# Kernel tuning notes

Hardware: AMD Instinct MI355X
Metric: run time of the kernel (lower is better)

The kernel has to match this reference:

```python
import jax, jax.numpy as jnp
import numpy as np

B, N, D, L, T = 64, 64, 128, 4, 10  # batch, atoms, hidden_dim, n_layers, n_atom_types
EPS = 1e-5


def setup_inputs() -> dict:
    key = jax.random.key(0)
    ks = jax.random.split(key, 10)
    def rn(k, shape, s=0.05):
        return jax.random.normal(k, shape, jnp.float32) * s
    return dict(
        positions=jax.random.normal(ks[0], (B, N, 3), jnp.float32),
        atomic_numbers=jax.random.randint(ks[1], (B, N), 0, T),
        embed=rn(ks[2], (T, D)),
        edge_w1=rn(ks[3], (L, 2 * D + 1, D)), edge_b1=jnp.zeros((L, D), jnp.float32),
        edge_w2=rn(ks[4], (L, D, D)), edge_b2=jnp.zeros((L, D), jnp.float32),
        node_w1=rn(ks[5], (L, 2 * D, D)), node_b1=jnp.zeros((L, D), jnp.float32),
        node_w2=rn(ks[6], (L, D, D)), node_b2=jnp.zeros((L, D), jnp.float32),
        ln_g=jnp.ones((L, D), jnp.float32), ln_b=jnp.zeros((L, D), jnp.float32),
        out_w=rn(ks[7], (D, 3)), out_b=jnp.zeros((3,), jnp.float32),
    )


def _layer(h, dist_sq, ew1, eb1, ew2, eb2, nw1, nb1, nw2, nb2, g, b):
    # edge_mlp first linear on cat([h_i, h_j, dist_sq]) == h@Wa (bcast over j)
    # + h@Wb (bcast over i) + dist_sq * w_d, avoiding materializing the concat.
    wa, wb, wd = ew1[:D], ew1[D:2 * D], ew1[2 * D]
    pre = (h @ wa)[:, :, None, :] + (h @ wb)[:, None, :, :] + dist_sq * wd + eb1  # [B,N,N,D]
    m_ij = jax.nn.silu(jax.nn.silu(pre) @ ew2 + eb2)
    m_i = m_ij.mean(axis=2)  # mean over j -> [B,N,D]
    # node_mlp on cat([h, m_i]) split the same way; dropout is eval-mode identity.
    h_out = jax.nn.silu(h @ nw1[:D] + m_i @ nw1[D:] + nb1) @ nw2 + nb2
    x = h + h_out
    mu = x.mean(-1, keepdims=True)
    var = ((x - mu) ** 2).mean(-1, keepdims=True)
    return (x - mu) / jnp.sqrt(var + EPS) * g + b


def reference(positions, atomic_numbers, embed, edge_w1, edge_b1, edge_w2, edge_b2,
              node_w1, node_b1, node_w2, node_b2, ln_g, ln_b, out_w, out_b):
    h = embed[atomic_numbers]  # [B,N,D]
    diff = positions[:, :, None, :] - positions[:, None, :, :]
    dist_sq = (diff ** 2).sum(-1, keepdims=True)  # [B,N,N,1]
    for i in range(L):
        h = _layer(h, dist_sq, edge_w1[i], edge_b1[i], edge_w2[i], edge_b2[i],
                   node_w1[i], node_b1[i], node_w2[i], node_b2[i], ln_g[i], ln_b[i])
    return h @ out_w + out_b  # [B,N,3]
```

## Files before the change

### kernel.cpp

```cpp
#include <hip/hip_runtime.h>
#include <hip/hip_fp16.h>


typedef _Float16 f16;
typedef _Float16 f16x4 __attribute__((ext_vector_type(4)));
typedef _Float16 f16x8 __attribute__((ext_vector_type(8)));
typedef float f32x4 __attribute__((ext_vector_type(4)));

union H2x4 { f16x8 v; __half2 h[4]; };

__device__ __forceinline__ float bf2f(unsigned short u) {
    union { unsigned int i; float f; } v; v.i = ((unsigned int)u) << 16; return v.f;
}
__device__ __forceinline__ unsigned short f2bf(float f) {
    union { float f; unsigned int i; } v; v.f = f;
    unsigned int x = v.i;
    return (unsigned short)((x + 0x7fffu + ((x >> 16) & 1u)) >> 16);
}
__device__ __forceinline__ float silu_f(float x) {
    float e = __builtin_amdgcn_exp2f(-1.44269504088896f * x);
    return x * __builtin_amdgcn_rcpf(1.0f + e);
}
__device__ __forceinline__ __half2 silu_h2(__half2 x, __half2 kf, __half2 one2) {
    __half2 e = h2exp2(__hmul2(x, kf));
    return __hmul2(x, h2rcp(__hadd2(one2, e)));
}

struct Ptrs { const void* p[14]; };

__device__ __forceinline__ float ldf(const void* p, int i, int bf) {
    return bf ? bf2f(((const unsigned short*)p)[i]) : ((const float*)p)[i];
}

#define FRAG_TOTAL 49152
#define ELEM_TOTAL 393216
#define SMALL_TOTAL 17539

__global__ __launch_bounds__(256) void prep_kernel(
    Ptrs ptrs, f16* dst, float* sc)
{
    __shared__ int flgsh;
    int t = threadIdx.x;
    if (t < 64) {
        int ex = (((const unsigned short*)ptrs.p[0])[t * 2] >> 7) & 0xFF;
        unsigned long long m = __ballot(ex >= 110 && ex <= 135);
        if (t == 0) flgsh = (__popcll(m) >= 40) ? 1 : 0;
    }
    __syncthreads();
    int bf = flgsh;

    int gid = blockIdx.x * 256 + t;
    if (gid < ELEM_TOTAL) {
        int f = gid >> 3, j = gid & 7;
        int lay = f / 12288;
        int r   = f % 12288;
        const void* src; int base, rowoff = 0, r2;
        if (r < 6144) {
            int mat = r >> 11; r2 = r & 2047;
            if (mat == 0)      { src = ptrs.p[2]; base = lay * 32896; }
            else if (mat == 1) { src = ptrs.p[2]; base = lay * 32896; rowoff = 128; }
            else               { src = ptrs.p[4]; base = lay * 16384; }
        } else if (r < 10240) {
            r2 = r - 6144; src = ptrs.p[6]; base = lay * 32768;
        } else {
            r2 = r - 10240; src = ptrs.p[8]; base = lay * 16384;
        }
        int s = r2 >> 9, c = (r2 >> 6) & 7, l = r2 & 63;
        int row = rowoff + s * 32 + ((l >> 4) << 3) + j;
        int col = (c << 4) + (l & 15);
        dst[gid] = (f16)ldf(src, base + row * 128 + col, bf);
    } else {
        int sid = gid - ELEM_TOTAL;
        if (sid >= SMALL_TOTAL) return;
        const void* src; int i;
        if      (sid < 12288) { src = ptrs.p[0]; i = sid; }
        else if (sid < 13568) { src = ptrs.p[1]; i = sid - 12288; }
        else if (sid < 14080) { int k = sid - 13568;
                                src = ptrs.p[2]; i = (k >> 7) * 32896 + 32768 + (k & 127); }
        else if (sid < 14592) { src = ptrs.p[3];  i = sid - 14080; }
        else if (sid < 15104) { src = ptrs.p[5];  i = sid - 14592; }
        else if (sid < 15616) { src = ptrs.p[7];  i = sid - 15104; }
        else if (sid < 16128) { src = ptrs.p[9];  i = sid - 15616; }
        else if (sid < 16640) { src = ptrs.p[10]; i = sid - 16128; }
        else if (sid < 17152) { src = ptrs.p[11]; i = sid - 16640; }
        else if (sid < 17536) { src = ptrs.p[12]; i = sid - 17152; }
        else                  { src = ptrs.p[13]; i = sid - 17536; }
        sc[sid] = ldf(src, i, bf);
    }
}

__global__ __launch_bounds__(512) void embed_ab_kernel(
    const int* an, const float* sc, const f16* wa, const f16* wb,
    const float* eb1C, f16* h16, f16* a16, f16* b16)
{
    int t = threadIdx.x;
    int w = t >> 6, lane = t & 63;
    int row0 = blockIdx.x << 4;
    int m_ = lane & 15, q_ = lane >> 4;
    const float* emb = sc + 12288;
    int a = an[row0 + m_];
    a = a < 0 ? 0 : (a > 9 ? 9 : a);
    f16x8 afrag[4];
#pragma unroll
    for (int s = 0; s < 4; s++) {
        f32x4 u0 = *(const f32x4*)(emb + a * 128 + s * 32 + q_ * 8);
        f32x4 u1 = *(const f32x4*)(emb + a * 128 + s * 32 + q_ * 8 + 4);
        f16x8 hv;
#pragma unroll
        for (int e = 0; e < 4; e++) { hv[e] = (f16)u0[e]; hv[e + 4] = (f16)u1[e]; }
        afrag[s] = hv;
        if (w == 0)
            *(f16x8*)(h16 + (row0 + m_) * 128 + s * 32 + q_ * 8) = hv;
    }
    int c = w;
#pragma unroll
    for (int mat = 0; mat < 2; mat++) {
        const f16* W = mat ? wb : wa;
        f16* out     = mat ? b16 : a16;
        float init = mat ? 0.0f : eb1C[c * 16 + m_];
        f32x4 acc = { init, init, init, init };
#pragma unroll
        for (int s = 0; s < 4; s++) {
            f16x8 bfr = *(const f16x8*)(W + ((s * 8 + c) * 64 + lane) * 8);
            acc = __builtin_amdgcn_mfma_f32_16x16x32_f16(afrag[s], bfr, acc, 0, 0, 0);
        }
#pragma unroll
        for (int r = 0; r < 4; r++)
            out[(row0 + q_ * 4 + r) * 128 + c * 16 + m_] = (f16)acc[r];
    }
}

__global__ __launch_bounds__(256) void edge_kernel(
    const float* sc, const f16* a16, const f16* b16,
    const f16* ew2_swz, const float* eb2C, const float* wdC, f16* m_out)
{
    __shared__ f16 Wlds[8192];
    __shared__ f16 S[64 * 136];
    __shared__ __half2 wd2_sh[64];
    __shared__ float dsq_sh[64];
    __shared__ float msum[256];

    int t  = threadIdx.x;
    int ig = blockIdx.x;
    int b  = ig >> 6;
    const float* posC = sc;
    int lane = t & 63, w = t >> 6;
    int wr = w & 1, wc = w >> 1;

#pragma unroll
    for (int k = 0; k < 4; k++) {
        int idx = (k * 256 + t) * 8;
        *(f16x8*)(Wlds + idx) = *(const f16x8*)(ew2_swz + idx);
    }
    f16x8 bfB[2][4];
#pragma unroll
    for (int s2 = 0; s2 < 2; s2++)
#pragma unroll
        for (int c = 0; c < 4; c++)
            bfB[s2][c] = *(const f16x8*)(ew2_swz +
                (((s2 + 2) * 8 + wc * 4 + c) * 64 + lane) * 8);

    if (t >= 64 && t < 128) {
        int u = t - 64;
        wd2_sh[u] = __floats2half2_rn(wdC[2 * u], wdC[2 * u + 1]);
    }
    if (t < 64) {
        float xi = posC[ig * 3 + 0], yi = posC[ig * 3 + 1], zi = posC[ig * 3 + 2];
        int jg = b * 64 + t;
        float dx = xi - posC[jg * 3 + 0];
        float dy = yi - posC[jg * 3 + 1];
        float dz = zi - posC[jg * 3 + 2];
        dsq_sh[t] = dx * dx + dy * dy + dz * dz;
    }
    __syncthreads();

    {
        int j  = t >> 2;
        int cb = (t & 3) * 32;
        float dsf = dsq_sh[j];
        __half dh = __float2half_rn(dsf);
        __half2 ds2 = __halves2half2(dh, dh);
        __half2 kf   = __floats2half2_rn(-1.44269504f, -1.44269504f);
        __half2 one2 = __floats2half2_rn(1.0f, 1.0f);
        H2x4 a_r[4], wd_r[4];
#pragma unroll
        for (int k = 0; k < 4; k++) {
            a_r[k].v  = *(const f16x8*)(a16 + ig * 128 + cb + k * 8);
            wd_r[k].v = *(const f16x8*)((const f16*)wd2_sh + cb + k * 8);
        }
#pragma unroll
        for (int k = 0; k < 4; k++) {
            H2x4 bv, sv;
            bv.v = *(const f16x8*)(b16 + (b * 64 + j) * 128 + cb + k * 8);
#pragma unroll
            for (int e = 0; e < 4; e++) {
                __half2 pre = __hfma2(ds2, wd_r[k].h[e],
                                      __hadd2(a_r[k].h[e], bv.h[e]));
                sv.h[e] = silu_h2(pre, kf, one2);
            }
            *(f16x8*)(S + j * 136 + cb + k * 8) = sv.v;
        }
    }
    __syncthreads();

    int m_ = lane & 15, q_ = lane >> 4;
    f32x4 acc[4][2];
#pragma unroll
    for (int c = 0; c < 4; c++) {
        float e = eb2C[(wc * 4 + c) * 16 + m_];
        acc[c][0] = (f32x4){ e, e, e, e };
        acc[c][1] = acc[c][0];
    }
#pragma unroll
    for (int s = 0; s < 2; s++) {
        f16x8 bfr[4];
#pragma unroll
        for (int c = 0; c < 4; c++)
            bfr[c] = *(const f16x8*)(Wlds + ((s * 8 + wc * 4 + c) * 64 + lane) * 8);
#pragma unroll
        for (int mb = 0; mb < 2; mb++) {
            f16x8 af = *(const f16x8*)(S + ((wr * 2 + mb) * 16 + m_) * 136 + s * 32 + q_ * 8);
#pragma unroll
            for (int c = 0; c < 4; c++)
                acc[c][mb] = __builtin_amdgcn_mfma_f32_16x16x32_f16(af, bfr[c], acc[c][mb], 0, 0, 0);
        }
    }
#pragma unroll
    for (int s2 = 0; s2 < 2; s2++) {
#pragma unroll
        for (int mb = 0; mb < 2; mb++) {
            f16x8 af = *(const f16x8*)(S + ((wr * 2 + mb) * 16 + m_) * 136 + (s2 + 2) * 32 + q_ * 8);
#pragma unroll
            for (int c = 0; c < 4; c++)
                acc[c][mb] = __builtin_amdgcn_mfma_f32_16x16x32_f16(af, bfB[s2][c], acc[c][mb], 0, 0, 0);
        }
    }
    float scv4[4];
#pragma unroll
    for (int c = 0; c < 4; c++) {
        float scv = 0.0f;
#pragma unroll
        for (int mb = 0; mb < 2; mb++)
#pragma unroll
            for (int r = 0; r < 4; r++)
                scv += silu_f(acc[c][mb][r]);
        scv += __shfl_xor(scv, 16);
        scv += __shfl_xor(scv, 32);
        scv4[c] = scv;
    }
    if (lane < 16) {
#pragma unroll
        for (int c = 0; c < 4; c++)
            msum[wr * 128 + (wc * 4 + c) * 16 + lane] = scv4[c];
    }
    __syncthreads();
    if (t < 128) {
        float mv = (msum[t] + msum[128 + t]) * (1.0f / 64.0f);
        m_out[ig * 128 + t] = (f16)mv;
    }
}

__global__ __launch_bounds__(512) void node_mid_kernel(
    const f16* h16, const f16* m16, const f16* nw1s, const f16* nw2s,
    const float* nb1C, const float* nb2C, const float* lngC, const float* lnbC,
    const f16* waN, const f16* wbN, const float* eb1N,
    f16* a16, f16* b16)
{
    __shared__ f16 relay[16 * 136];
    __shared__ float s1sh[8][16], s2sh[8][16];
    int t = threadIdx.x;
    int w = t >> 6, lane = t & 63;
    int row0 = blockIdx.x << 4;
    int m_ = lane & 15, q_ = lane >> 4;
    int c = w;

    f16x8 af[8];
#pragma unroll
    for (int s = 0; s < 4; s++) {
        af[s]     = *(const f16x8*)(h16 + (row0 + m_) * 128 + s * 32 + q_ * 8);
        af[s + 4] = *(const f16x8*)(m16 + (row0 + m_) * 128 + s * 32 + q_ * 8);
    }
    {
        float e = nb1C[c * 16 + m_];
        f32x4 acc = { e, e, e, e };
#pragma unroll
        for (int s = 0; s < 8; s++) {
            f16x8 bfr = *(const f16x8*)(nw1s + ((s * 8 + c) * 64 + lane) * 8);
            acc = __builtin_amdgcn_mfma_f32_16x16x32_f16(af[s], bfr, acc, 0, 0, 0);
        }
#pragma unroll
        for (int r = 0; r < 4; r++)
            relay[(q_ * 4 + r) * 136 + c * 16 + m_] = (f16)silu_f(acc[r]);
    }
    __syncthreads();
    f16x8 uf[4];
#pragma unroll
    for (int s = 0; s < 4; s++)
        uf[s] = *(const f16x8*)(relay + m_ * 136 + s * 32 + q_ * 8);
    float x[4];
    {
        float e = nb2C[c * 16 + m_];
        f32x4 acc = { e, e, e, e };
#pragma unroll
        for (int s = 0; s < 4; s++) {
            f16x8 bfr = *(const f16x8*)(nw2s + ((s * 8 + c) * 64 + lane) * 8);
            acc = __builtin_amdgcn_mfma_f32_16x16x32_f16(uf[s], bfr, acc, 0, 0, 0);
        }
#pragma unroll
        for (int r = 0; r < 4; r++)
            x[r] = acc[r] + (float)h16[(row0 + q_ * 4 + r) * 128 + c * 16 + m_];
    }
    float s1p[4], s2p[4];
#pragma unroll
    for (int r = 0; r < 4; r++) {
        s1p[r] = x[r];
        s2p[r] = x[r] * x[r];
    }
#pragma unroll
    for (int msk = 1; msk < 16; msk <<= 1)
#pragma unroll
        for (int r = 0; r < 4; r++) {
            s1p[r] += __shfl_xor(s1p[r], msk);
            s2p[r] += __shfl_xor(s2p[r], msk);
        }
    if (m_ == 0)
#pragma unroll
        for (int r = 0; r < 4; r++) {
            s1sh[w][q_ * 4 + r] = s1p[r];
            s2sh[w][q_ * 4 + r] = s2p[r];
        }
    __syncthreads();
    float mu[4], rs[4];
#pragma unroll
    for (int r = 0; r < 4; r++) {
        int row = q_ * 4 + r;
        float S1 = 0.0f, S2 = 0.0f;
#pragma unroll
        for (int w2 = 0; w2 < 8; w2++) { S1 += s1sh[w2][row]; S2 += s2sh[w2][row]; }
        mu[r] = S1 * (1.0f / 128.0f);
        float var = S2 * (1.0f / 128.0f) - mu[r] * mu[r];
        rs[r] = rsqrtf(var + 1e-5f);
    }
#pragma unroll
    for (int r = 0; r < 4; r++) {
        int col = c * 16 + m_;
        int row = row0 + q_ * 4 + r;
        float y = (x[r] - mu[r]) * rs[r] * lngC[col] + lnbC[col];
        ((f16*)h16)[row * 128 + col] = (f16)y;
        relay[(q_ * 4 + r) * 136 + col] = (f16)y;
    }
    __syncthreads();
    f16x8 hf[4];
#pragma unroll
    for (int s = 0; s < 4; s++)
        hf[s] = *(const f16x8*)(relay + m_ * 136 + s * 32 + q_ * 8);
#pragma unroll
    for (int mat = 0; mat < 2; mat++) {
        const f16* W = mat ? wbN : waN;
        f16* out     = mat ? b16 : a16;
        float init = mat ? 0.0f : eb1N[c * 16 + m_];
        f32x4 acc = { init, init, init, init };
#pragma unroll
        for (int s = 0; s < 4; s++) {
            f16x8 bfr = *(const f16x8*)(W + ((s * 8 + c) * 64 + lane) * 8);
            acc = __builtin_amdgcn_mfma_f32_16x16x32_f16(hf[s], bfr, acc, 0, 0, 0);
        }
#pragma unroll
        for (int r = 0; r < 4; r++)
            out[(row0 + q_ * 4 + r) * 128 + c * 16 + m_] = (f16)acc[r];
    }
}

__global__ __launch_bounds__(512) void node_final_kernel(
    const void* pos_raw, const f16* h16, const f16* m16,
    const f16* nw1s, const f16* nw2s,
    const float* nb1C, const float* nb2C, const float* lngC, const float* lnbC,
    const float* owC, const float* obC, void* out)
{
    __shared__ f16 relay[16 * 136];
    __shared__ float s1sh[8][16], s2sh[8][16];
    __shared__ float psh[8][16][3];
    __shared__ int flgsh;
    int t = threadIdx.x;
    int w = t >> 6, lane = t & 63;
    int row0 = blockIdx.x << 4;
    int m_ = lane & 15, q_ = lane >> 4;
    int c = w;

    if (t < 64) {
        int ex = (((const unsigned short*)pos_raw)[t * 2] >> 7) & 0xFF;
        unsigned long long mk = __ballot(ex >= 110 && ex <= 135);
        if (t == 0) flgsh = (__popcll(mk) >= 40) ? 1 : 0;
    }

    f16x8 af[8];
#pragma unroll
    for (int s = 0; s < 4; s++) {
        af[s]     = *(const f16x8*)(h16 + (row0 + m_) * 128 + s * 32 + q_ * 8);
        af[s + 4] = *(const f16x8*)(m16 + (row0 + m_) * 128 + s * 32 + q_ * 8);
    }
    {
        float e = nb1C[c * 16 + m_];
        f32x4 acc = { e, e, e, e };
#pragma unroll
        for (int s = 0; s < 8; s++) {
            f16x8 bfr = *(const f16x8*)(nw1s + ((s * 8 + c) * 64 + lane) * 8);
            acc = __builtin_amdgcn_mfma_f32_16x16x32_f16(af[s], bfr, acc, 0, 0, 0);
        }
#pragma unroll
        for (int r = 0; r < 4; r++)
            relay[(q_ * 4 + r) * 136 + c * 16 + m_] = (f16)silu_f(acc[r]);
    }
    __syncthreads();
    f16x8 uf[4];
#pragma unroll
    for (int s = 0; s < 4; s++)
        uf[s] = *(const f16x8*)(relay + m_ * 136 + s * 32 + q_ * 8);
    float x[4];
    {
        float e = nb2C[c * 16 + m_];
        f32x4 acc = { e, e, e, e };
#pragma unroll
        for (int s = 0; s < 4; s++) {
            f16x8 bfr = *(const f16x8*)(nw2s + ((s * 8 + c) * 64 + lane) * 8);
            acc = __builtin_amdgcn_mfma_f32_16x16x32_f16(uf[s], bfr, acc, 0, 0, 0);
        }
#pragma unroll
        for (int r = 0; r < 4; r++)
            x[r] = acc[r] + (float)h16[(row0 + q_ * 4 + r) * 128 + c * 16 + m_];
    }
    float s1p[4], s2p[4];
#pragma unroll
    for (int r = 0; r < 4; r++) {
        s1p[r] = x[r];
        s2p[r] = x[r] * x[r];
    }
#pragma unroll
    for (int msk = 1; msk < 16; msk <<= 1)
#pragma unroll
        for (int r = 0; r < 4; r++) {
            s1p[r] += __shfl_xor(s1p[r], msk);
            s2p[r] += __shfl_xor(s2p[r], msk);
        }
    if (m_ == 0)
#pragma unroll
        for (int r = 0; r < 4; r++) {
            s1sh[w][q_ * 4 + r] = s1p[r];
            s2sh[w][q_ * 4 + r] = s2p[r];
        }
    __syncthreads();
    float p[3][4];
#pragma unroll
    for (int r = 0; r < 4; r++) {
        int row = q_ * 4 + r;
        float S1 = 0.0f, S2 = 0.0f;
#pragma unroll
        for (int w2 = 0; w2 < 8; w2++) { S1 += s1sh[w2][row]; S2 += s2sh[w2][row]; }
        float mu = S1 * (1.0f / 128.0f);
        float var = S2 * (1.0f / 128.0f) - mu * mu;
        float rs = rsqrtf(var + 1e-5f);
        int col = c * 16 + m_;
        float y = (x[r] - mu) * rs * lngC[col] + lnbC[col];
        p[0][r] = y * owC[col * 3 + 0];
        p[1][r] = y * owC[col * 3 + 1];
        p[2][r] = y * owC[col * 3 + 2];
    }
#pragma unroll
    for (int msk = 1; msk < 16; msk <<= 1)
#pragma unroll
        for (int k = 0; k < 3; k++)
#pragma unroll
            for (int r = 0; r < 4; r++)
                p[k][r] += __shfl_xor(p[k][r], msk);
    if (m_ == 0)
#pragma unroll
        for (int r = 0; r < 4; r++)
#pragma unroll
            for (int k = 0; k < 3; k++)
                psh[w][q_ * 4 + r][k] = p[k][r];
    __syncthreads();
    if (t < 16) {
        int row = row0 + t;
        int bf = flgsh;
#pragma unroll
        for (int k = 0; k < 3; k++) {
            float v = obC[k];
#pragma unroll
            for (int w2 = 0; w2 < 8; w2++) v += psh[w2][t][k];
            if (bf) ((unsigned short*)out)[row * 3 + k] = f2bf(v);
            else    ((float*)out)[row * 3 + k] = v;
        }
    }
}

extern "C" void kernel_launch(void* const* d_in, const int* in_sizes, int n_in,
                              void* d_out, int out_size, void* d_ws, size_t ws_size,
                              hipStream_t stream)
{
    const int* an = (const int*)d_in[1];

    char* ws = (char*)d_ws;
    float* sc   = (float*)(ws + 1024);
    f16*   Wswz = (f16*)(ws + (128u << 10));
    f16*   h16  = (f16*)(ws + (1u << 20));
    f16*   a16  = (f16*)(ws + (2u << 20));
    f16*   b16  = (f16*)(ws + (3u << 20));
    f16*   m16  = (f16*)(ws + (4u << 20));

    Ptrs ptrs;
    const int src_idx[14] = {0, 2, 3, 4, 5, 6, 7, 8, 9, 10, 11, 12, 13, 14};
    for (int k = 0; k < 14; k++) ptrs.p[k] = d_in[src_idx[k]];

    prep_kernel<<<1605, 256, 0, stream>>>(ptrs, Wswz, sc);
    embed_ab_kernel<<<256, 512, 0, stream>>>(an, sc, Wswz, Wswz + 16384,
                                             sc + 14080, h16, a16, b16);
    for (int lay = 0; lay < 4; lay++) {
        const f16* wl = Wswz + lay * 98304;
        const float* wdC  = sc + 13568 + lay * 128;
        const float* eb2C = sc + 14592 + lay * 128;
        const float* nb1C = sc + 15104 + lay * 128;
        const float* nb2C = sc + 15616 + lay * 128;
        const float* lngC = sc + 16128 + lay * 128;
        const float* lnbC = sc + 16640 + lay * 128;

        edge_kernel<<<4096, 256, 0, stream>>>(sc, a16, b16, wl + 32768,
                                              eb2C, wdC, m16);
        if (lay < 3) {
            const f16* wlN = Wswz + (lay + 1) * 98304;
            node_mid_kernel<<<256, 512, 0, stream>>>(
                h16, m16, wl + 49152, wl + 81920, nb1C, nb2C, lngC, lnbC,
                wlN, wlN + 16384, sc + 14080 + (lay + 1) * 128, a16, b16);
        } else {
            node_final_kernel<<<256, 512, 0, stream>>>(
                d_in[0], h16, m16, wl + 49152, wl + 81920,
                nb1C, nb2C, lngC, lnbC,
                sc + 17152, sc + 17536, d_out);
        }
    }
}
```

Baseline: 216.0 us.

## Fuse embed, edge, and node layers into one persistent kernel with per-batch flags

Replaces the embed, per-layer edge, and node kernels with a single 256-block persistent kernel. Each block owns 16 rows of one molecule and runs all four layers, keeping h, a, and m in LDS. Blocks of the same batch exchange the b projection through double-buffered global memory and synchronise with atomic per-batch flags. This removes eight kernel launches and the global round trips for m/h/a, but edge work drops from 4096 blocks to 256 blocks, which lowers parallelism and adds spin-wait synchronisation between co-resident blocks.

```diff
diff --git a/kernel.cpp b/kernel.cpp
--- a/kernel.cpp
+++ b/kernel.cpp
@@ -3,7 +3,6 @@
 
 
 typedef _Float16 f16;
-typedef _Float16 f16x4 __attribute__((ext_vector_type(4)));
 typedef _Float16 f16x8 __attribute__((ext_vector_type(8)));
 typedef float f32x4 __attribute__((ext_vector_type(4)));
 
@@ -32,15 +31,15 @@
     return bf ? bf2f(((const unsigned short*)p)[i]) : ((const float*)p)[i];
 }
 
-#define FRAG_TOTAL 49152
 #define ELEM_TOTAL 393216
 #define SMALL_TOTAL 17539
 
 __global__ __launch_bounds__(256) void prep_kernel(
-    Ptrs ptrs, f16* dst, float* sc)
+    Ptrs ptrs, f16* dst, float* sc, int* flags)
 {
     __shared__ int flgsh;
     int t = threadIdx.x;
+    if (blockIdx.x == 0 && t < 64) flags[t] = 0;
     if (t < 64) {
         int ex = (((const unsigned short*)ptrs.p[0])[t * 2] >> 7) & 0xFF;
         unsigned long long m = __ballot(ex >= 110 && ex <= 135);
@@ -89,452 +88,325 @@
     }
 }
 
-__global__ __launch_bounds__(512) void embed_ab_kernel(
-    const int* an, const float* sc, const f16* wa, const f16* wb,
-    const float* eb1C, f16* h16, f16* a16, f16* b16)
+__global__ __launch_bounds__(512) void net_kernel(
+    const void* pos_raw, const int* an, const float* sc, const f16* Wswz,
+    f16* b0, f16* b1, int* flags, void* out)
 {
+    __shared__ f16 S[2][64 * 136];
+    __shared__ f16 a_lds[16 * 136];
+    __shared__ f16 h_lds[16 * 136];
+    __shared__ f16 m_lds[16 * 136];
+    __shared__ __half dsq2[16][64];
+    __shared__ __half2 wd2_sh[64];
+    __shared__ float s1sh[8][16], s2sh[8][16];
+    __shared__ int flgsh;
+
     int t = threadIdx.x;
     int w = t >> 6, lane = t & 63;
-    int row0 = blockIdx.x << 4;
-    int m_ = lane & 15, q_ = lane >> 4;
-    const float* emb = sc + 12288;
-    int a = an[row0 + m_];
-    a = a < 0 ? 0 : (a > 9 ? 9 : a);
-    f16x8 afrag[4];
-#pragma unroll
-    for (int s = 0; s < 4; s++) {
-        f32x4 u0 = *(const f32x4*)(emb + a * 128 + s * 32 + q_ * 8);
-        f32x4 u1 = *(const f32x4*)(emb + a * 128 + s * 32 + q_ * 8 + 4);
-        f16x8 hv;
-#pragma unroll
-        for (int e = 0; e < 4; e++) { hv[e] = (f16)u0[e]; hv[e + 4] = (f16)u1[e]; }
-        afrag[s] = hv;
-        if (w == 0)
-            *(f16x8*)(h16 + (row0 + m_) * 128 + s * 32 + q_ * 8) = hv;
-    }
-    int c = w;
-#pragma unroll
-    for (int mat = 0; mat < 2; mat++) {
-        const f16* W = mat ? wb : wa;
-        f16* out     = mat ? b16 : a16;
-        float init = mat ? 0.0f : eb1C[c * 16 + m_];
-        f32x4 acc = { init, init, init, init };
-#pragma unroll
-        for (int s = 0; s < 4; s++) {
-            f16x8 bfr = *(const f16x8*)(W + ((s * 8 + c) * 64 + lane) * 8);
-            acc = __builtin_amdgcn_mfma_f32_16x16x32_f16(afrag[s], bfr, acc, 0, 0, 0);
-        }
-#pragma unroll
-        for (int r = 0; r < 4; r++)
-            out[(row0 + q_ * 4 + r) * 128 + c * 16 + m_] = (f16)acc[r];
-    }
-}
-
-__global__ __launch_bounds__(256) void edge_kernel(
-    const float* sc, const f16* a16, const f16* b16,
-    const f16* ew2_swz, const float* eb2C, const float* wdC, f16* m_out)
-{
-    __shared__ f16 Wlds[8192];
-    __shared__ f16 S[64 * 136];
-    __shared__ __half2 wd2_sh[64];
-    __shared__ float dsq_sh[64];
-    __shared__ float msum[256];
-
-    int t  = threadIdx.x;
-    int ig = blockIdx.x;
-    int b  = ig >> 6;
-    const float* posC = sc;
-    int lane = t & 63, w = t >> 6;
-    int wr = w & 1, wc = w >> 1;
-
-#pragma unroll
-    for (int k = 0; k < 4; k++) {
-        int idx = (k * 256 + t) * 8;
-        *(f16x8*)(Wlds + idx) = *(const f16x8*)(ew2_swz + idx);
-    }
-    f16x8 bfB[2][4];
-#pragma unroll
-    for (int s2 = 0; s2 < 2; s2++)
-#pragma unroll
-        for (int c = 0; c < 4; c++)
-            bfB[s2][c] = *(const f16x8*)(ew2_swz +
-                (((s2 + 2) * 8 + wc * 4 + c) * 64 + lane) * 8);
-
-    if (t >= 64 && t < 128) {
-        int u = t - 64;
-        wd2_sh[u] = __floats2half2_rn(wdC[2 * u], wdC[2 * u + 1]);
-    }
-    if (t < 64) {
-        float xi = posC[ig * 3 + 0], yi = posC[ig * 3 + 1], zi = posC[ig * 3 + 2];
-        int jg = b * 64 + t;
-        float dx = xi - posC[jg * 3 + 0];
-        float dy = yi - posC[jg * 3 + 1];
-        float dz = zi - posC[jg * 3 + 2];
-        dsq_sh[t] = dx * dx + dy * dy + dz * dz;
-    }
-    __syncthreads();
-
-    {
-        int j  = t >> 2;
-        int cb = (t & 3) * 32;
-        float dsf = dsq_sh[j];
-        __half dh = __float2half_rn(dsf);
-        __half2 ds2 = __halves2half2(dh, dh);
-        __half2 kf   = __floats2half2_rn(-1.44269504f, -1.44269504f);
-        __half2 one2 = __floats2half2_rn(1.0f, 1.0f);
-        H2x4 a_r[4], wd_r[4];
-#pragma unroll
-        for (int k = 0; k < 4; k++) {
-            a_r[k].v  = *(const f16x8*)(a16 + ig * 128 + cb + k * 8);
-            wd_r[k].v = *(const f16x8*)((const f16*)wd2_sh + cb + k * 8);
-        }
-#pragma unroll
-        for (int k = 0; k < 4; k++) {
-            H2x4 bv, sv;
-            bv.v = *(const f16x8*)(b16 + (b * 64 + j) * 128 + cb + k * 8);
-#pragma unroll
-            for (int e = 0; e < 4; e++) {
-                __half2 pre = __hfma2(ds2, wd_r[k].h[e],
-                                      __hadd2(a_r[k].h[e], bv.h[e]));
-                sv.h[e] = silu_h2(pre, kf, one2);
-            }
-            *(f16x8*)(S + j * 136 + cb + k * 8) = sv.v;
-        }
-    }
-    __syncthreads();
-
-    int m_ = lane & 15, q_ = lane >> 4;
-    f32x4 acc[4][2];
-#pragma unroll
-    for (int c = 0; c < 4; c++) {
-        float e = eb2C[(wc * 4 + c) * 16 + m_];
-        acc[c][0] = (f32x4){ e, e, e, e };
-        acc[c][1] = acc[c][0];
-    }
-#pragma unroll
-    for (int s = 0; s < 2; s++) {
-        f16x8 bfr[4];
-#pragma unroll
-        for (int c = 0; c < 4; c++)
-            bfr[c] = *(const f16x8*)(Wlds + ((s * 8 + wc * 4 + c) * 64 + lane) * 8);
-#pragma unroll
-        for (int mb = 0; mb < 2; mb++) {
-            f16x8 af = *(const f16x8*)(S + ((wr * 2 + mb) * 16 + m_) * 136 + s * 32 + q_ * 8);
-#pragma unroll
-            for (int c = 0; c < 4; c++)
-                acc[c][mb] = __builtin_amdgcn_mfma_f32_16x16x32_f16(af, bfr[c], acc[c][mb], 0, 0, 0);
-        }
-    }
-#pragma unroll
-    for (int s2 = 0; s2 < 2; s2++) {
-#pragma unroll
-        for (int mb = 0; mb < 2; mb++) {
-            f16x8 af = *(const f16x8*)(S + ((wr * 2 + mb) * 16 + m_) * 136 + (s2 + 2) * 32 + q_ * 8);
-#pragma unroll
-            for (int c = 0; c < 4; c++)
-                acc[c][mb] = __builtin_amdgcn_mfma_f32_16x16x32_f16(af, bfB[s2][c], acc[c][mb], 0, 0, 0);
-        }
-    }
-    float scv4[4];
-#pragma unroll
-    for (int c = 0; c < 4; c++) {
-        float scv = 0.0f;
-#pragma unroll
-        for (int mb = 0; mb < 2; mb++)
-#pragma unroll
-            for (int r = 0; r < 4; r++)
-                scv += silu_f(acc[c][mb][r]);
-        scv += __shfl_xor(scv, 16);
-        scv += __shfl_xor(scv, 32);
-        scv4[c] = scv;
-    }
-    if (lane < 16) {
-#pragma unroll
-        for (int c = 0; c < 4; c++)
-            msum[wr * 128 + (wc * 4 + c) * 16 + lane] = scv4[c];
-    }
-    __syncthreads();
-    if (t < 128) {
-        float mv = (msum[t] + msum[128 + t]) * (1.0f / 64.0f);
-        m_out[ig * 128 + t] = (f16)mv;
-    }
-}
-
-__global__ __launch_bounds__(512) void node_mid_kernel(
-    const f16* h16, const f16* m16, const f16* nw1s, const f16* nw2s,
-    const float* nb1C, const float* nb2C, const float* lngC, const float* lnbC,
-    const f16* waN, const f16* wbN, const float* eb1N,
-    f16* a16, f16* b16)
-{
-    __shared__ f16 relay[16 * 136];
-    __shared__ float s1sh[8][16], s2sh[8][16];
-    int t = threadIdx.x;
-    int w = t >> 6, lane = t & 63;
-    int row0 = blockIdx.x << 4;
     int m_ = lane & 15, q_ = lane >> 4;
     int c = w;
-
-    f16x8 af[8];
-#pragma unroll
-    for (int s = 0; s < 4; s++) {
-        af[s]     = *(const f16x8*)(h16 + (row0 + m_) * 128 + s * 32 + q_ * 8);
-        af[s + 4] = *(const f16x8*)(m16 + (row0 + m_) * 128 + s * 32 + q_ * 8);
-    }
-    {
-        float e = nb1C[c * 16 + m_];
-        f32x4 acc = { e, e, e, e };
-#pragma unroll
-        for (int s = 0; s < 8; s++) {
-            f16x8 bfr = *(const f16x8*)(nw1s + ((s * 8 + c) * 64 + lane) * 8);
-            acc = __builtin_amdgcn_mfma_f32_16x16x32_f16(af[s], bfr, acc, 0, 0, 0);
-        }
-#pragma unroll
-        for (int r = 0; r < 4; r++)
-            relay[(q_ * 4 + r) * 136 + c * 16 + m_] = (f16)silu_f(acc[r]);
-    }
-    __syncthreads();
-    f16x8 uf[4];
-#pragma unroll
-    for (int s = 0; s < 4; s++)
-        uf[s] = *(const f16x8*)(relay + m_ * 136 + s * 32 + q_ * 8);
-    float x[4];
-    {
-        float e = nb2C[c * 16 + m_];
-        f32x4 acc = { e, e, e, e };
-#pragma unroll
-        for (int s = 0; s < 4; s++) {
-            f16x8 bfr = *(const f16x8*)(nw2s + ((s * 8 + c) * 64 + lane) * 8);
-            acc = __builtin_amdgcn_mfma_f32_16x16x32_f16(uf[s], bfr, acc, 0, 0, 0);
-        }
-#pragma unroll
-        for (int r = 0; r < 4; r++)
-            x[r] = acc[r] + (float)h16[(row0 + q_ * 4 + r) * 128 + c * 16 + m_];
-    }
-    float s1p[4], s2p[4];
-#pragma unroll
-    for (int r = 0; r < 4; r++) {
-        s1p[r] = x[r];
-        s2p[r] = x[r] * x[r];
-    }
-#pragma unroll
-    for (int msk = 1; msk < 16; msk <<= 1)
-#pragma unroll
-        for (int r = 0; r < 4; r++) {
-            s1p[r] += __shfl_xor(s1p[r], msk);
-            s2p[r] += __shfl_xor(s2p[r], msk);
-        }
-    if (m_ == 0)
-#pragma unroll
-        for (int r = 0; r < 4; r++) {
-            s1sh[w][q_ * 4 + r] = s1p[r];
-            s2sh[w][q_ * 4 + r] = s2p[r];
-        }
-    __syncthreads();
-    float mu[4], rs[4];
-#pragma unroll
-    for (int r = 0; r < 4; r++) {
-        int row = q_ * 4 + r;
-        float S1 = 0.0f, S2 = 0.0f;
-#pragma unroll
-        for (int w2 = 0; w2 < 8; w2++) { S1 += s1sh[w2][row]; S2 += s2sh[w2][row]; }
-        mu[r] = S1 * (1.0f / 128.0f);
-        float var = S2 * (1.0f / 128.0f) - mu[r] * mu[r];
-        rs[r] = rsqrtf(var + 1e-5f);
-    }
-#pragma unroll
-    for (int r = 0; r < 4; r++) {
-        int col = c * 16 + m_;
-        int row = row0 + q_ * 4 + r;
-        float y = (x[r] - mu[r]) * rs[r] * lngC[col] + lnbC[col];
-        ((f16*)h16)[row * 128 + col] = (f16)y;
-        relay[(q_ * 4 + r) * 136 + col] = (f16)y;
-    }
-    __syncthreads();
-    f16x8 hf[4];
-#pragma unroll
-    for (int s = 0; s < 4; s++)
-        hf[s] = *(const f16x8*)(relay + m_ * 136 + s * 32 + q_ * 8);
-#pragma unroll
-    for (int mat = 0; mat < 2; mat++) {
-        const f16* W = mat ? wbN : waN;
-        f16* out     = mat ? b16 : a16;
-        float init = mat ? 0.0f : eb1N[c * 16 + m_];
-        f32x4 acc = { init, init, init, init };
-#pragma unroll
-        for (int s = 0; s < 4; s++) {
-            f16x8 bfr = *(const f16x8*)(W + ((s * 8 + c) * 64 + lane) * 8);
-            acc = __builtin_amdgcn_mfma_f32_16x16x32_f16(hf[s], bfr, acc, 0, 0, 0);
-        }
-#pragma unroll
-        for (int r = 0; r < 4; r++)
-            out[(row0 + q_ * 4 + r) * 128 + c * 16 + m_] = (f16)acc[r];
-    }
-}
-
-__global__ __launch_bounds__(512) void node_final_kernel(
-    const void* pos_raw, const f16* h16, const f16* m16,
-    const f16* nw1s, const f16* nw2s,
-    const float* nb1C, const float* nb2C, const float* lngC, const float* lnbC,
-    const float* owC, const float* obC, void* out)
-{
-    __shared__ f16 relay[16 * 136];
-    __shared__ float s1sh[8][16], s2sh[8][16];
-    __shared__ float psh[8][16][3];
-    __shared__ int flgsh;
-    int t = threadIdx.x;
-    int w = t >> 6, lane = t & 63;
-    int row0 = blockIdx.x << 4;
-    int m_ = lane & 15, q_ = lane >> 4;
-    int c = w;
+    int b  = blockIdx.x >> 2;
+    int r0 = b * 64 + (blockIdx.x & 3) * 16;
+    const float* posC = sc;
 
     if (t < 64) {
         int ex = (((const unsigned short*)pos_raw)[t * 2] >> 7) & 0xFF;
         unsigned long long mk = __ballot(ex >= 110 && ex <= 135);
         if (t == 0) flgsh = (__popcll(mk) >= 40) ? 1 : 0;
     }
-
-    f16x8 af[8];
-#pragma unroll
-    for (int s = 0; s < 4; s++) {
-        af[s]     = *(const f16x8*)(h16 + (row0 + m_) * 128 + s * 32 + q_ * 8);
-        af[s + 4] = *(const f16x8*)(m16 + (row0 + m_) * 128 + s * 32 + q_ * 8);
-    }
+    for (int k = t; k < 1024; k += 512) {
+        int ii = k >> 6, j = k & 63;
+        int gi = r0 + ii, gj = b * 64 + j;
+        float dx = posC[gi * 3 + 0] - posC[gj * 3 + 0];
+        float dy = posC[gi * 3 + 1] - posC[gj * 3 + 1];
+        float dz = posC[gi * 3 + 2] - posC[gj * 3 + 2];
+        dsq2[ii][j] = __float2half_rn(dx * dx + dy * dy + dz * dz);
+    }
+
     {
-        float e = nb1C[c * 16 + m_];
-        f32x4 acc = { e, e, e, e };
-#pragma unroll
-        for (int s = 0; s < 8; s++) {
-            f16x8 bfr = *(const f16x8*)(nw1s + ((s * 8 + c) * 64 + lane) * 8);
-            acc = __builtin_amdgcn_mfma_f32_16x16x32_f16(af[s], bfr, acc, 0, 0, 0);
-        }
-#pragma unroll
-        for (int r = 0; r < 4; r++)
-            relay[(q_ * 4 + r) * 136 + c * 16 + m_] = (f16)silu_f(acc[r]);
+        const float* emb  = sc + 12288;
+        const float* eb1C = sc + 14080;
+        int a = an[r0 + m_];
+        a = a < 0 ? 0 : (a > 9 ? 9 : a);
+        f16x8 afrag[4];
+#pragma unroll
+        for (int s = 0; s < 4; s++) {
+            f32x4 u0 = *(const f32x4*)(emb + a * 128 + s * 32 + q_ * 8);
+            f32x4 u1 = *(const f32x4*)(emb + a * 128 + s * 32 + q_ * 8 + 4);
+            f16x8 hv;
+#pragma unroll
+            for (int e = 0; e < 4; e++) { hv[e] = (f16)u0[e]; hv[e + 4] = (f16)u1[e]; }
+            afrag[s] = hv;
+            if (w == 0)
+                *(f16x8*)(h_lds + m_ * 136 + s * 32 + q_ * 8) = hv;
+        }
+#pragma unroll
+        for (int mat = 0; mat < 2; mat++) {
+            const f16* W = mat ? (Wswz + 16384) : Wswz;
+            float init = mat ? 0.0f : eb1C[c * 16 + m_];
+            f32x4 acc = { init, init, init, init };
+#pragma unroll
+            for (int s = 0; s < 4; s++) {
+                f16x8 bfv = *(const f16x8*)(W + ((s * 8 + c) * 64 + lane) * 8);
+                acc = __builtin_amdgcn_mfma_f32_16x16x32_f16(afrag[s], bfv, acc, 0, 0, 0);
+            }
+#pragma unroll
+            for (int r = 0; r < 4; r++) {
+                if (mat == 0)
+                    a_lds[(q_ * 4 + r) * 136 + c * 16 + m_] = (f16)acc[r];
+                else
+                    b0[(r0 + q_ * 4 + r) * 128 + c * 16 + m_] = (f16)acc[r];
+            }
+        }
     }
     __syncthreads();
-    f16x8 uf[4];
-#pragma unroll
-    for (int s = 0; s < 4; s++)
-        uf[s] = *(const f16x8*)(relay + m_ * 136 + s * 32 + q_ * 8);
-    float x[4];
-    {
-        float e = nb2C[c * 16 + m_];
-        f32x4 acc = { e, e, e, e };
-#pragma unroll
-        for (int s = 0; s < 4; s++) {
-            f16x8 bfr = *(const f16x8*)(nw2s + ((s * 8 + c) * 64 + lane) * 8);
-            acc = __builtin_amdgcn_mfma_f32_16x16x32_f16(uf[s], bfr, acc, 0, 0, 0);
-        }
-#pragma unroll
-        for (int r = 0; r < 4; r++)
-            x[r] = acc[r] + (float)h16[(row0 + q_ * 4 + r) * 128 + c * 16 + m_];
-    }
-    float s1p[4], s2p[4];
-#pragma unroll
-    for (int r = 0; r < 4; r++) {
-        s1p[r] = x[r];
-        s2p[r] = x[r] * x[r];
-    }
-#pragma unroll
-    for (int msk = 1; msk < 16; msk <<= 1)
-#pragma unroll
-        for (int r = 0; r < 4; r++) {
-            s1p[r] += __shfl_xor(s1p[r], msk);
-            s2p[r] += __shfl_xor(s2p[r], msk);
-        }
-    if (m_ == 0)
-#pragma unroll
-        for (int r = 0; r < 4; r++) {
-            s1sh[w][q_ * 4 + r] = s1p[r];
-            s2sh[w][q_ * 4 + r] = s2p[r];
-        }
-    __syncthreads();
-    float p[3][4];
-#pragma unroll
-    for (int r = 0; r < 4; r++) {
-        int row = q_ * 4 + r;
-        float S1 = 0.0f, S2 = 0.0f;
-#pragma unroll
-        for (int w2 = 0; w2 < 8; w2++) { S1 += s1sh[w2][row]; S2 += s2sh[w2][row]; }
-        float mu = S1 * (1.0f / 128.0f);
-        float var = S2 * (1.0f / 128.0f) - mu * mu;
-        float rs = rsqrtf(var + 1e-5f);
-        int col = c * 16 + m_;
-        float y = (x[r] - mu) * rs * lngC[col] + lnbC[col];
-        p[0][r] = y * owC[col * 3 + 0];
-        p[1][r] = y * owC[col * 3 + 1];
-        p[2][r] = y * owC[col * 3 + 2];
-    }
-#pragma unroll
-    for (int msk = 1; msk < 16; msk <<= 1)
-#pragma unroll
-        for (int k = 0; k < 3; k++)
-#pragma unroll
-            for (int r = 0; r < 4; r++)
-                p[k][r] += __shfl_xor(p[k][r], msk);
-    if (m_ == 0)
-#pragma unroll
-        for (int r = 0; r < 4; r++)
-#pragma unroll
-            for (int k = 0; k < 3; k++)
-                psh[w][q_ * 4 + r][k] = p[k][r];
-    __syncthreads();
-    if (t < 16) {
-        int row = row0 + t;
-        int bf = flgsh;
-#pragma unroll
-        for (int k = 0; k < 3; k++) {
-            float v = obC[k];
-#pragma unroll
-            for (int w2 = 0; w2 < 8; w2++) v += psh[w2][t][k];
-            if (bf) ((unsigned short*)out)[row * 3 + k] = f2bf(v);
-            else    ((float*)out)[row * 3 + k] = v;
-        }
-    }
-}
-
-extern "C" void kernel_launch(void* const* d_in, const int* in_sizes, int n_in,
-                              void* d_out, int out_size, void* d_ws, size_t ws_size,
-                              hipStream_t stream)
-{
-    const int* an = (const int*)d_in[1];
-
-    char* ws = (char*)d_ws;
-    float* sc   = (float*)(ws + 1024);
-    f16*   Wswz = (f16*)(ws + (128u << 10));
-    f16*   h16  = (f16*)(ws + (1u << 20));
-    f16*   a16  = (f16*)(ws + (2u << 20));
-    f16*   b16  = (f16*)(ws + (3u << 20));
-    f16*   m16  = (f16*)(ws + (4u << 20));
-
-    Ptrs ptrs;
-    const int src_idx[14] = {0, 2, 3, 4, 5, 6, 7, 8, 9, 10, 11, 12, 13, 14};
-    for (int k = 0; k < 14; k++) ptrs.p[k] = d_in[src_idx[k]];
-
-    prep_kernel<<<1605, 256, 0, stream>>>(ptrs, Wswz, sc);
-    embed_ab_kernel<<<256, 512, 0, stream>>>(an, sc, Wswz, Wswz + 16384,
-                                             sc + 14080, h16, a16, b16);
+    if (t == 0) {
+        __threadfence();
+        __hip_atomic_fetch_add(&flags[b], 1, __ATOMIC_RELEASE,
+                               __HIP_MEMORY_SCOPE_AGENT);
+    }
+
     for (int lay = 0; lay < 4; lay++) {
-        const f16* wl = Wswz + lay * 98304;
+        const f16* wl   = Wswz + lay * 98304;
+        const f16* ew2s = wl + 32768;
+        const f16* nw1s = wl + 49152;
+        const f16* nw2s = wl + 81920;
         const float* wdC  = sc + 13568 + lay * 128;
         const float* eb2C = sc + 14592 + lay * 128;
         const float* nb1C = sc + 15104 + lay * 128;
         const float* nb2C = sc + 15616 + lay * 128;
         const float* lngC = sc + 16128 + lay * 128;
         const float* lnbC = sc + 16640 + lay * 128;
-
-        edge_kernel<<<4096, 256, 0, stream>>>(sc, a16, b16, wl + 32768,
-                                              eb2C, wdC, m16);
+        const f16* bcur = (lay & 1) ? b1 : b0;
+        f16*       bnxt = (lay & 1) ? b0 : b1;
+
+        if (t == 0) {
+            int target = 4 * (lay + 1);
+            int spins = 0;
+            while (__hip_atomic_load(&flags[b], __ATOMIC_ACQUIRE,
+                                     __HIP_MEMORY_SCOPE_AGENT) < target) {
+                __builtin_amdgcn_s_sleep(8);
+                if (++spins > (1 << 20)) break;
+            }
+        }
+        __syncthreads();
+
+        if (t < 64) wd2_sh[t] = __floats2half2_rn(wdC[2 * t], wdC[2 * t + 1]);
+        f16x8 bfr[4];
+#pragma unroll
+        for (int s = 0; s < 4; s++)
+            bfr[s] = *(const f16x8*)(ew2s + ((s * 8 + c) * 64 + lane) * 8);
+        __syncthreads();
+
+        float eb2v = eb2C[c * 16 + m_];
+        const __half2 kf   = __floats2half2_rn(-1.44269504f, -1.44269504f);
+        const __half2 one2 = __floats2half2_rn(1.0f, 1.0f);
+        for (int i = 0; i < 16; i++) {
+            f16* Sc = S[i & 1];
+#pragma unroll
+            for (int k = 0; k < 2; k++) {
+                int chunk = t + 512 * k;
+                int row = chunk >> 4, col = (chunk & 15) * 8;
+                __half dh = dsq2[i][row];
+                __half2 ds2 = __halves2half2(dh, dh);
+                H2x4 av, bv, wv, sv;
+                av.v = *(const f16x8*)(a_lds + i * 136 + col);
+                bv.v = *(const f16x8*)(bcur + (b * 64 + row) * 128 + col);
+                wv.v = *(const f16x8*)((const f16*)wd2_sh + col);
+#pragma unroll
+                for (int e = 0; e < 4; e++) {
+                    __half2 pre = __hfma2(ds2, wv.h[e], __hadd2(av.h[e], bv.h[e]));
+                    sv.h[e] = silu_h2(pre, kf, one2);
+                }
+                *(f16x8*)(Sc + row * 136 + col) = sv.v;
+            }
+            __syncthreads();
+            f32x4 acc[4];
+#pragma unroll
+            for (int mb = 0; mb < 4; mb++) acc[mb] = (f32x4){ eb2v, eb2v, eb2v, eb2v };
+#pragma unroll
+            for (int s = 0; s < 4; s++)
+#pragma unroll
+                for (int mb = 0; mb < 4; mb++) {
+                    f16x8 af = *(const f16x8*)(Sc + (mb * 16 + m_) * 136 + s * 32 + q_ * 8);
+                    acc[mb] = __builtin_amdgcn_mfma_f32_16x16x32_f16(af, bfr[s], acc[mb], 0, 0, 0);
+                }
+            float scv = 0.0f;
+#pragma unroll
+            for (int mb = 0; mb < 4; mb++)
+#pragma unroll
+                for (int r = 0; r < 4; r++)
+                    scv += silu_f(acc[mb][r]);
+            scv += __shfl_xor(scv, 16);
+            scv += __shfl_xor(scv, 32);
+            if (lane < 16)
+                m_lds[i * 136 + c * 16 + lane] = (f16)(scv * (1.0f / 64.0f));
+        }
+        __syncthreads();
+
+        f16x8 af2[8];
+#pragma unroll
+        for (int s = 0; s < 4; s++) {
+            af2[s]     = *(const f16x8*)(h_lds + m_ * 136 + s * 32 + q_ * 8);
+            af2[s + 4] = *(const f16x8*)(m_lds + m_ * 136 + s * 32 + q_ * 8);
+        }
+        f16* relay = &S[0][0];
+        {
+            float e = nb1C[c * 16 + m_];
+            f32x4 acc = { e, e, e, e };
+#pragma unroll
+            for (int s = 0; s < 8; s++) {
+                f16x8 bv = *(const f16x8*)(nw1s + ((s * 8 + c) * 64 + lane) * 8);
+                acc = __builtin_amdgcn_mfma_f32_16x16x32_f16(af2[s], bv, acc, 0, 0, 0);
+            }
+#pragma unroll
+            for (int r = 0; r < 4; r++)
+                relay[(q_ * 4 + r) * 136 + c * 16 + m_] = (f16)silu_f(acc[r]);
+        }
+        __syncthreads();
+        f16x8 uf[4];
+#pragma unroll
+        for (int s = 0; s < 4; s++)
+            uf[s] = *(const f16x8*)(relay + m_ * 136 + s * 32 + q_ * 8);
+        float x[4];
+        {
+            float e = nb2C[c * 16 + m_];
+            f32x4 acc = { e, e, e, e };
+#pragma unroll
+            for (int s = 0; s < 4; s++) {
+                f16x8 bv = *(const f16x8*)(nw2s + ((s * 8 + c) * 64 + lane) * 8);
+                acc = __builtin_amdgcn_mfma_f32_16x16x32_f16(uf[s], bv, acc, 0, 0, 0);
+            }
+#pragma unroll
+            for (int r = 0; r < 4; r++)
+                x[r] = acc[r] + (float)h_lds[(q_ * 4 + r) * 136 + c * 16 + m_];
+        }
+        float s1p[4], s2p[4];
+#pragma unroll
+        for (int r = 0; r < 4; r++) { s1p[r] = x[r]; s2p[r] = x[r] * x[r]; }
+#pragma unroll
+        for (int msk = 1; msk < 16; msk <<= 1)
+#pragma unroll
+            for (int r = 0; r < 4; r++) {
+                s1p[r] += __shfl_xor(s1p[r], msk);
+                s2p[r] += __shfl_xor(s2p[r], msk);
+            }
+        if (m_ == 0)
+#pragma unroll
+            for (int r = 0; r < 4; r++) {
+                s1sh[w][q_ * 4 + r] = s1p[r];
+                s2sh[w][q_ * 4 + r] = s2p[r];
+            }
+        __syncthreads();
+        float mu[4], rs[4];
+#pragma unroll
+        for (int r = 0; r < 4; r++) {
+            int row = q_ * 4 + r;
+            float S1 = 0.0f, S2 = 0.0f;
+#pragma unroll
+            for (int w2 = 0; w2 < 8; w2++) { S1 += s1sh[w2][row]; S2 += s2sh[w2][row]; }
+            mu[r] = S1 * (1.0f / 128.0f);
+            float var = S2 * (1.0f / 128.0f) - mu[r] * mu[r];
+            rs[r] = rsqrtf(var + 1e-5f);
+        }
+
         if (lay < 3) {
+#pragma unroll
+            for (int r = 0; r < 4; r++) {
+                int col = c * 16 + m_;
+                float y = (x[r] - mu[r]) * rs[r] * lngC[col] + lnbC[col];
+                h_lds[(q_ * 4 + r) * 136 + col] = (f16)y;
+            }
+            __syncthreads();
+            f16x8 hf[4];
+#pragma unroll
+            for (int s = 0; s < 4; s++)
+                hf[s] = *(const f16x8*)(h_lds + m_ * 136 + s * 32 + q_ * 8);
             const f16* wlN = Wswz + (lay + 1) * 98304;
-            node_mid_kernel<<<256, 512, 0, stream>>>(
-                h16, m16, wl + 49152, wl + 81920, nb1C, nb2C, lngC, lnbC,
-                wlN, wlN + 16384, sc + 14080 + (lay + 1) * 128, a16, b16);
+            const float* eb1N = sc + 14080 + (lay + 1) * 128;
+#pragma unroll
+            for (int mat = 0; mat < 2; mat++) {
+                const f16* W = mat ? (wlN + 16384) : wlN;
+                float init = mat ? 0.0f : eb1N[c * 16 + m_];
+                f32x4 acc = { init, init, init, init };
+#pragma unroll
+                for (int s = 0; s < 4; s++) {
+                    f16x8 bv = *(const f16x8*)(W + ((s * 8 + c) * 64 + lane) * 8);
+                    acc = __builtin_amdgcn_mfma_f32_16x16x32_f16(hf[s], bv, acc, 0, 0, 0);
+                }
+#pragma unroll
+                for (int r = 0; r < 4; r++) {
+                    if (mat == 0)
+                        a_lds[(q_ * 4 + r) * 136 + c * 16 + m_] = (f16)acc[r];
+                    else
+                        bnxt[(r0 + q_ * 4 + r) * 128 + c * 16 + m_] = (f16)acc[r];
+                }
+            }
+            __syncthreads();
+            if (t == 0) {
+                __threadfence();
+                __hip_atomic_fetch_add(&flags[b], 1, __ATOMIC_RELEASE,
+                                       __HIP_MEMORY_SCOPE_AGENT);
+            }
         } else {
-            node_final_kernel<<<256, 512, 0, stream>>>(
-                d_in[0], h16, m16, wl + 49152, wl + 81920,
-                nb1C, nb2C, lngC, lnbC,
-                sc + 17152, sc + 17536, d_out);
-        }
-    }
-}
+            const float* owC = sc + 17152;
+            const float* obC = sc + 17536;
+            float (*psh)[16][3] = (float (*)[16][3])(void*)dsq2;
+            float p[3][4];
+#pragma unroll
+            for (int r = 0; r < 4; r++) {
+                int col = c * 16 + m_;
+                float y = (x[r] - mu[r]) * rs[r] * lngC[col] + lnbC[col];
+                p[0][r] = y * owC[col * 3 + 0];
+                p[1][r] = y * owC[col * 3 + 1];
+                p[2][r] = y * owC[col * 3 + 2];
+            }
+#pragma unroll
+            for (int msk = 1; msk < 16; msk <<= 1)
+#pragma unroll
+                for (int k = 0; k < 3; k++)
+#pragma unroll
+                    for (int r = 0; r < 4; r++)
+                        p[k][r] += __shfl_xor(p[k][r], msk);
+            if (m_ == 0)
+#pragma unroll
+                for (int r = 0; r < 4; r++)
+#pragma unroll
+                    for (int k = 0; k < 3; k++)
+                        psh[w][q_ * 4 + r][k] = p[k][r];
+            __syncthreads();
+            if (t < 16) {
+                int row = r0 + t;
+                int bf = flgsh;
+#pragma unroll
+                for (int k = 0; k < 3; k++) {
+                    float v = obC[k];
+#pragma unroll
+                    for (int w2 = 0; w2 < 8; w2++) v += psh[w2][t][k];
+                    if (bf) ((unsigned short*)out)[row * 3 + k] = f2bf(v);
+                    else    ((float*)out)[row * 3 + k] = v;
+                }
+            }
+        }
+    }
+}
+
+extern "C" void kernel_launch(void* const* d_in, const int* in_sizes, int n_in,
+                              void* d_out, int out_size, void* d_ws, size_t ws_size,
+                              hipStream_t stream)
+{
+    char* ws = (char*)d_ws;
+    int*   flags = (int*)ws;
+    float* sc    = (float*)(ws + 1024);
+    f16*   Wswz  = (f16*)(ws + (128u << 10));
+    f16*   b0    = (f16*)(ws + (1u << 20));
+    f16*   b1    = (f16*)(ws + (2u << 20));
+
+    Ptrs ptrs;
+    const int src_idx[14] = {0, 2, 3, 4, 5, 6, 7, 8, 9, 10, 11, 12, 13, 14};
+    for (int k = 0; k < 14; k++) ptrs.p[k] = d_in[src_idx[k]];
+
+    prep_kernel<<<1605, 256, 0, stream>>>(ptrs, Wswz, sc, flags);
+    net_kernel<<<256, 512, 0, stream>>>(d_in[0], (const int*)d_in[1],
+                                        sc, Wswz, b0, b1, flags, d_out);
+}
```

New measurement: 257.6 us. 19.3% more time.
